# Optimization experiments

Measured on AMD Instinct MI355X. Metric: run time of the kernel, lower is better.

Reference implementation:

```python
import jax, jax.numpy as jnp
import numpy as np

B, NX, NT, W, M = 4, 512, 128, 64, 16
EPS = 1e-5


def setup_inputs() -> dict:
    key = jax.random.key(0)
    ks = jax.random.split(key, 13)
    scale = 1.0 / (W * W)  # torch: scale * torch.rand(..., cfloat) -> U[0,1) real & imag
    return {
        "x": jax.random.normal(ks[0], (B, NX, NT, W), jnp.float32),
        "grid": jnp.linspace(0.0, 1.0, NX, dtype=jnp.float32),
        "pole_re": scale * jax.random.uniform(ks[1], (W, W, M), jnp.float32),
        "pole_im": scale * jax.random.uniform(ks[2], (W, W, M), jnp.float32),
        "res_re": scale * jax.random.uniform(ks[3], (W, W, M), jnp.float32),
        "res_im": scale * jax.random.uniform(ks[4], (W, W, M), jnp.float32),
        "conv_w": jax.random.normal(ks[5], (W, W), jnp.float32) / np.sqrt(W),
        "conv_b": jax.random.normal(ks[6], (W,), jnp.float32) * 0.02,
        "gru_Wx": jax.random.normal(ks[7], (3 * W, W), jnp.float32) / np.sqrt(W),
        "gru_Wh": jax.random.normal(ks[8], (3 * W, W), jnp.float32) / np.sqrt(W),
        "gru_bx": jax.random.normal(ks[9], (3 * W,), jnp.float32) * 0.02,
        "gru_bh": jax.random.normal(ks[10], (3 * W,), jnp.float32) * 0.02,
        "out_W": jax.random.normal(ks[11], (W, W), jnp.float32) / np.sqrt(W),
        "out_b": jax.random.normal(ks[12], (W,), jnp.float32) * 0.02,
    }


def instance_norm(v):
    # torch InstanceNorm1d (affine=False, biased var) over last dim; v: [N, C, L]
    mu = v.mean(-1, keepdims=True)
    var = ((v - mu) ** 2).mean(-1, keepdims=True)
    return (v - mu) * jax.lax.rsqrt(var + EPS)


def pr_forward(xs, grid, pole, residue):
    # xs: [BT, W, Nx]; pole/residue: [in, out, modes] complex64
    nx = xs.shape[-1]
    dt = grid[1] - grid[0]
    alpha = jnp.fft.fft(xs)  # [BT, W, Nx] complex64
    lam = 1j * (2.0 * np.pi) * jnp.fft.fftfreq(nx, dt).astype(jnp.float32)  # [Nx]
    Hw = residue / (lam[:, None, None, None] - pole)  # [Nx, i, o, m]
    or1 = jnp.einsum('bix,xiom->box', alpha, Hw)       # [BT, W, Nx]
    or2 = -jnp.einsum('bix,xiom->bom', alpha, Hw)      # [BT, W, M]
    x1 = jnp.real(jnp.fft.ifft(or1, n=nx))
    # exp of outer product pole (x) grid: [i, o, m, Nx]
    term2 = jnp.exp(pole[..., None] * grid.astype(jnp.complex64)[None, None, None, :])
    # faithful to torch einsum 'bix,ioxz->boz': or2 channel contracts with term2's in-dim
    x2 = jnp.real(jnp.einsum('bim,iomz->boz', or2, term2)) / nx
    return x1 + x2


def gru(xseq, Wx, Wh, bx, bh):
    # xseq: [N, T, D] -> [N, T, H]; torch nn.GRU gate order (r, z, n)
    H = Wh.shape[1]
    gx = xseq @ Wx.T + bx  # precompute input gates [N, T, 3H]

    def step(h, g):
        gh = h @ Wh.T + bh
        xr, xz, xn = jnp.split(g, 3, axis=-1)
        hr, hz, hn = jnp.split(gh, 3, axis=-1)
        r = jax.nn.sigmoid(xr + hr)
        z = jax.nn.sigmoid(xz + hz)
        n = jnp.tanh(xn + r * hn)
        h = (1.0 - z) * n + z * h
        return h, h

    h0 = jnp.zeros((xseq.shape[0], H), xseq.dtype)
    _, hs = jax.lax.scan(step, h0, gx.transpose(1, 0, 2))
    return hs.transpose(1, 0, 2)


def reference(x, grid, pole_re, pole_im, res_re, res_im, conv_w, conv_b,
              gru_Wx, gru_Wh, gru_bx, gru_bh, out_W, out_b):
    b, nx, nt, w = x.shape
    xs = x.transpose(0, 2, 3, 1).reshape(b * nt, w, nx)  # [B*Nt, W, Nx]
    pole = pole_re + 1j * pole_im
    residue = res_re + 1j * res_im
    x1 = instance_norm(pr_forward(instance_norm(xs), grid, pole, residue))
    x2 = jnp.einsum('oi,bin->bon', conv_w, xs) + conv_b[None, :, None]  # Conv1d k=1
    h = jnp.sin(x1 + x2)
    h = h.reshape(b, nt, w, nx).transpose(0, 3, 1, 2).reshape(b * nx, nt, w)
    y = gru(h, gru_Wx, gru_Wh, gru_bx, gru_bh) @ out_W.T + out_b
    return y.reshape(b, nx, nt, w)
```

## Files before the change

### kernel.cpp

```cpp
#include <hip/hip_runtime.h>
#include <math.h>

#define PI2F 6.283185307179586f


__global__ __launch_bounds__(256) void k1a_transpose(const float* __restrict__ x,
                                                     float* __restrict__ xs) {
  const int bt = blockIdx.x >> 2, nt4 = blockIdx.x & 3;
  const int b = bt >> 7, t = bt & 127;
  const int n0 = nt4 * 128;
  __shared__ float tile[128 * 66];
  const int tid = threadIdx.x;
  const int i = tid & 63, nq = tid >> 6;
  const float* xb = x + (size_t)b * 4194304 + (size_t)t * 64;
  for (int k = 0; k < 32; k++) {
    int nl = nq + 4 * k;
    tile[nl * 66 + i] = xb[(size_t)(n0 + nl) * 8192 + i];
  }
  __syncthreads();
  float* dst = xs + (size_t)bt * 32768;
  for (int idx = tid; idx < 8192; idx += 256) {
    int ii = idx >> 7, nl = idx & 127;
    dst[ii * 512 + n0 + nl] = tile[nl * 66 + ii];
  }
}

__global__ __launch_bounds__(64) void k2_fft(const float* __restrict__ xs,
                                             float2* __restrict__ alpha,
                                             float2* __restrict__ a0,
                                             float2* __restrict__ a256,
                                             float2* __restrict__ s1o,
                                             float2* __restrict__ s2o,
                                             const float* __restrict__ grd) {
  __shared__ float2 bufA[512], bufB[512], tw[256];
  const int s = blockIdx.x, tid = threadIdx.x;
  const float dt = grd[1] - grd[0];
  const float Ndt = 512.f * dt;
  for (int m = tid; m < 256; m += 64) {
    float ang = -PI2F * (float)m * (1.f / 512.f);
    float sv, cv; sincosf(ang, &sv, &cv);
    tw[m].x = cv; tw[m].y = sv;
  }
  const float* src = xs + (size_t)s * 512;
  float v[8]; float sm = 0.f, sq = 0.f;
#pragma unroll
  for (int k = 0; k < 8; k++) { v[k] = src[tid + 64 * k]; sm += v[k]; sq += v[k] * v[k]; }
#pragma unroll
  for (int off = 32; off; off >>= 1) { sm += __shfl_down(sm, off); sq += __shfl_down(sq, off); }
  sm = __shfl(sm, 0); sq = __shfl(sq, 0);
  float mu = sm * (1.f / 512.f);
  float var = sq * (1.f / 512.f) - mu * mu;
  float rs = rsqrtf(var + 1e-5f);
#pragma unroll
  for (int k = 0; k < 8; k++) { bufA[tid + 64 * k].x = (v[k] - mu) * rs; bufA[tid + 64 * k].y = 0.f; }
  __syncthreads();
  float2* sp = bufA; float2* dp = bufB;
  int Ns = 1;
  for (int st = 0; st < 9; st++) {
    const int shift = 8 - st;
    for (int jj = 0; jj < 4; jj++) {
      int j = tid + 64 * jj;
      int r = j & (Ns - 1);
      float2 a = sp[j], b = sp[j + 256];
      float2 w = tw[r << shift];
      float wbx = w.x * b.x - w.y * b.y;
      float wby = w.x * b.y + w.y * b.x;
      int id = ((j >> st) << (st + 1)) + r;
      dp[id].x = a.x + wbx; dp[id].y = a.y + wby;
      dp[id + Ns].x = a.x - wbx; dp[id + Ns].y = a.y - wby;
    }
    __syncthreads();
    float2* tp = sp; sp = dp; dp = tp;
    Ns <<= 1;
  }
  float2* dst = alpha + (size_t)s * 256;
  float s1x = 0.f, s1y = 0.f, s2x = 0.f, s2y = 0.f;
  for (int k = tid; k < 512; k += 64) {
    float2 vv = sp[k];
    if (k < 256) dst[k] = vv;
    if (k != 0) {
      int kk = (k < 256) ? k : k - 512;
      float invL = Ndt / (PI2F * (float)kk);
      s1x += vv.y * invL; s1y -= vv.x * invL;
      float invL2 = invL * invL;
      s2x -= vv.x * invL2; s2y -= vv.y * invL2;
    }
  }
#pragma unroll
  for (int off = 32; off; off >>= 1) {
    s1x += __shfl_down(s1x, off); s1y += __shfl_down(s1y, off);
    s2x += __shfl_down(s2x, off); s2y += __shfl_down(s2y, off);
  }
  if (tid == 0) {
    s1o[s].x = s1x; s1o[s].y = s1y;
    s2o[s].x = s2x; s2o[s].y = s2y;
    a0[s] = sp[0];
    a256[s] = sp[256];
  }
}

__global__ __launch_bounds__(64) void k3a_R(const float* __restrict__ pre, const float* __restrict__ pim,
                                            const float* __restrict__ rre, const float* __restrict__ rim,
                                            float2* __restrict__ R0, float2* __restrict__ R1,
                                            float2* __restrict__ R2,
                                            float* __restrict__ Pm, float* __restrict__ Qm,
                                            float* __restrict__ ptr_re, float* __restrict__ ptr_im) {
  const int i = blockIdx.x, o = threadIdx.x;
  float r0x = 0, r0y = 0, r1x = 0, r1y = 0, r2x = 0, r2y = 0;
  for (int m = 0; m < 16; m++) {
    size_t idx = ((size_t)i * 64 + o) * 16 + m;
    float px = pre[idx], py = pim[idx];
    float rx = rre[idx], ry = rim[idx];
    r1x += rx; r1y += ry;
    r2x += rx * px - ry * py; r2y += rx * py + ry * px;
    float inv = 1.f / (px * px + py * py);
    r0x -= (rx * px + ry * py) * inv;
    r0y -= (ry * px - rx * py) * inv;
    ptr_re[((size_t)i * 16 + m) * 64 + o] = px;
    ptr_im[((size_t)i * 16 + m) * 64 + o] = py;
  }
  R0[i * 64 + o].x = r0x; R0[i * 64 + o].y = r0y;
  R1[i * 64 + o].x = r1x; R1[i * 64 + o].y = r1y;
  R2[i * 64 + o].x = r2x; R2[i * 64 + o].y = r2y;
  Pm[i * 64 + o] = 2.f * r1x;
  Qm[i * 64 + o] = 2.f * r2x;
}

__global__ __launch_bounds__(1024) void k3b_or2(const float* __restrict__ pre, const float* __restrict__ pim,
                                                const float* __restrict__ rre, const float* __restrict__ rim,
                                                const float2* __restrict__ a0, const float2* __restrict__ s1,
                                                const float2* __restrict__ s2, float2* __restrict__ or2) {
  const int bt = blockIdx.x;
  __shared__ float2 A0[64], S1[64], S2[64];
  const int tid = threadIdx.x;
  if (tid < 64) { A0[tid] = a0[bt * 64 + tid]; S1[tid] = s1[bt * 64 + tid]; S2[tid] = s2[bt * 64 + tid]; }
  __syncthreads();
  float ax = 0.f, ay = 0.f;
  for (int i = 0; i < 64; i++) {
    size_t idx = (size_t)i * 1024 + tid;
    float px = pre[idx], py = pim[idx];
    float rx = rre[idx], ry = rim[idx];
    float inv = 1.f / (px * px + py * py);
    float q0x = -(rx * px + ry * py) * inv;
    float q0y = -(ry * px - rx * py) * inv;
    float2 a0v = A0[i], s1v = S1[i], s2v = S2[i];
    float tx = q0x * a0v.x - q0y * a0v.y + rx * s1v.x - ry * s1v.y;
    float ty = q0x * a0v.y + q0y * a0v.x + rx * s1v.y + ry * s1v.x;
    float rpx = rx * px - ry * py, rpy = rx * py + ry * px;
    tx += rpx * s2v.x - rpy * s2v.y;
    ty += rpx * s2v.y + rpy * s2v.x;
    ax -= tx; ay -= ty;
  }
  or2[(size_t)bt * 1024 + tid].x = ax;
  or2[(size_t)bt * 1024 + tid].y = ay;
}

__global__ __launch_bounds__(256) void k3c_T(const float2* __restrict__ or2,
                                             const float* __restrict__ ptr_re, const float* __restrict__ ptr_im,
                                             const float2* __restrict__ R0, const float2* __restrict__ R1,
                                             const float2* __restrict__ R2,
                                             const float2* __restrict__ a0, const float2* __restrict__ a256,
                                             float* __restrict__ T0, float* __restrict__ T1,
                                             float* __restrict__ T2,
                                             float* __restrict__ or10re, float* __restrict__ r256o,
                                             const float* __restrict__ grd) {
  const int bt = blockIdx.x * 4 + (threadIdx.x >> 6);
  const int o = threadIdx.x & 63;
  const float dt = grd[1] - grd[0];
  const float invL256 = -(512.f * dt) / (PI2F * 256.f);
  float ox = 0.f;
  float c1x = 0.f, c1y = 0.f, c2x = 0.f, c2y = 0.f;
  for (int i = 0; i < 64; i++) {
    float2 av = a0[bt * 64 + i];
    float2 rv = R0[i * 64 + o];
    ox += av.x * rv.x - av.y * rv.y;
    float2 aw = a256[bt * 64 + i];
    float2 r1v = R1[i * 64 + o], r2v = R2[i * 64 + o];
    c1x += aw.x * r1v.x - aw.y * r1v.y;
    c1y += aw.x * r1v.y + aw.y * r1v.x;
    c2x += aw.x * r2v.x - aw.y * r2v.y;
    c2y += aw.x * r2v.y + aw.y * r2v.x;
  }
  or10re[bt * 64 + o] = ox;
  r256o[bt * 64 + o] = invL256 * (c1y - invL256 * c2x);
  float t0 = 0.f, t1 = 0.f, t2 = 0.f;
  for (int im = 0; im < 1024; im++) {
    float2 c = or2[(size_t)bt * 1024 + im];
    float px = ptr_re[(size_t)im * 64 + o], py = ptr_im[(size_t)im * 64 + o];
    t0 += c.x;
    t1 += c.x * px - c.y * py;
    float p2x = px * px - py * py, p2y = 2.f * px * py;
    t2 += c.x * p2x - c.y * p2y;
  }
  T1[bt * 64 + o] = t1; T2[bt * 64 + o] = t2;
  if (o == 0) T0[bt] = t0;
}

__global__ __launch_bounds__(256) void k4_or1(float2* __restrict__ alpha,
                                              const float* __restrict__ Pm, const float* __restrict__ Qm,
                                              const float* __restrict__ or10re, const float* __restrict__ r256o,
                                              const float* __restrict__ grd) {
  const int bt = blockIdx.x >> 2, xc = blockIdx.x & 3;
  const int x0 = xc * 64;
  __shared__ float aRe[64][68], aIm[64][68];
  const int tid = threadIdx.x;
  const float dt = grd[1] - grd[0];
  const float Ndt = 512.f * dt;
  float2* base = alpha + (size_t)bt * 16384;
  for (int idx = tid; idx < 4096; idx += 256) {
    int ii = idx >> 6, xl = idx & 63;
    float2 v = base[ii * 256 + x0 + xl];
    aRe[ii][xl] = v.x; aIm[ii][xl] = v.y;
  }
  __syncthreads();
  const int xq = tid & 15, oq = tid >> 4;
  const int xb = xq * 4, ob = oq * 4;
  float c1r[4][4] = {}, c1i[4][4] = {}, c2r[4][4] = {}, c2i[4][4] = {};
#pragma unroll 4
  for (int i = 0; i < 64; i++) {
    float4 ar = *(const float4*)&aRe[i][xb];
    float4 ai = *(const float4*)&aIm[i][xb];
    float4 pv = *(const float4*)&Pm[i * 64 + ob];
    float4 qv = *(const float4*)&Qm[i * 64 + ob];
    float pa[4] = {pv.x, pv.y, pv.z, pv.w};
    float qa[4] = {qv.x, qv.y, qv.z, qv.w};
    float arr[4] = {ar.x, ar.y, ar.z, ar.w};
    float aii[4] = {ai.x, ai.y, ai.z, ai.w};
#pragma unroll
    for (int a = 0; a < 4; a++) {
#pragma unroll
      for (int c = 0; c < 4; c++) {
        c1r[a][c] += arr[c] * pa[a];
        c1i[a][c] += aii[c] * pa[a];
        c2r[a][c] += arr[c] * qa[a];
        c2i[a][c] += aii[c] * qa[a];
      }
    }
  }
#pragma unroll
  for (int a = 0; a < 4; a++) {
    int o = ob + a;
    float2* orow = base + o * 256 + x0;
#pragma unroll
    for (int c = 0; c < 4; c++) {
      int gx = x0 + xb + c;
      float re, im;
      if (gx == 0) {
        re = or10re[bt * 64 + o];
        im = r256o[bt * 64 + o];
      } else {
        float invL = Ndt / (PI2F * (float)gx);
        re = invL * (c1i[a][c] - invL * c2r[a][c]);
        im = -invL * (c1r[a][c] + invL * c2i[a][c]);
      }
      orow[xb + c].x = re; orow[xb + c].y = im;
    }
  }
}

__global__ __launch_bounds__(64) void k5_ifft(const float2* __restrict__ G,
                                              float* __restrict__ x1,
                                              const float* __restrict__ T0, const float* __restrict__ T1,
                                              const float* __restrict__ T2, const float* __restrict__ grd) {
  __shared__ float2 bufA[512], bufB[512], tw[256];
  const int s = blockIdx.x, tid = threadIdx.x;
  const int bt = s >> 6;
  for (int m = tid; m < 256; m += 64) {
    float ang = PI2F * (float)m * (1.f / 512.f);
    float sv, cv; sincosf(ang, &sv, &cv);
    tw[m].x = cv; tw[m].y = sv;
  }
  const float2* src = G + (size_t)s * 256;
  float2 g0 = src[0];
  for (int k = tid; k < 512; k += 64) {
    float2 vv; vv.x = 0.f; vv.y = 0.f;
    if (k >= 1 && k < 256) vv = src[k];
    bufA[k] = vv;
  }
  __syncthreads();
  float2* sp = bufA; float2* dp = bufB;
  int Ns = 1;
  for (int st = 0; st < 9; st++) {
    const int shift = 8 - st;
    for (int jj = 0; jj < 4; jj++) {
      int j = tid + 64 * jj;
      int r = j & (Ns - 1);
      float2 a = sp[j], b = sp[j + 256];
      float2 w = tw[r << shift];
      float wbx = w.x * b.x - w.y * b.y;
      float wby = w.x * b.y + w.y * b.x;
      int id = ((j >> st) << (st + 1)) + r;
      dp[id].x = a.x + wbx; dp[id].y = a.y + wby;
      dp[id + Ns].x = a.x - wbx; dp[id + Ns].y = a.y - wby;
    }
    __syncthreads();
    float2* tp = sp; sp = dp; dp = tp;
    Ns <<= 1;
  }
  const float t0 = T0[bt], t1 = T1[s], t2 = T2[s];
  float* dst = x1 + (size_t)s * 512;
  for (int k = tid; k < 512; k += 64) {
    float g = grd[k];
    float sgn = (k & 1) ? -1.f : 1.f;
    dst[k] = (sp[k].x + g0.x + sgn * g0.y + t0 + t1 * g + 0.5f * t2 * g * g) * (1.f / 512.f);
  }
}

__global__ __launch_bounds__(256) void k6a_stats(const float* __restrict__ x1,
                                                 float* __restrict__ mu2, float* __restrict__ rs2) {
  const int row = blockIdx.x * 4 + (threadIdx.x >> 6);
  const int lane = threadIdx.x & 63;
  const float* p = x1 + (size_t)row * 512;
  float s = 0.f, s2 = 0.f;
#pragma unroll
  for (int k = 0; k < 8; k++) { float v = p[lane + 64 * k]; s += v; s2 += v * v; }
#pragma unroll
  for (int off = 32; off; off >>= 1) { s += __shfl_down(s, off); s2 += __shfl_down(s2, off); }
  if (lane == 0) {
    float mu = s * (1.f / 512.f);
    float var = s2 * (1.f / 512.f) - mu * mu;
    mu2[row] = mu;
    rs2[row] = rsqrtf(var + 1e-5f);
  }
}

__global__ __launch_bounds__(256) void k6b_assemble(const float* __restrict__ xsraw,
                                                    const float* __restrict__ x1,
                                                    const float* __restrict__ conv_w,
                                                    const float* __restrict__ conv_b,
                                                    const float* __restrict__ mu2, const float* __restrict__ rs2,
                                                    float* __restrict__ hseq) {
  const int bt = blockIdx.x >> 2, nt4 = blockIdx.x & 3;
  const int b = bt >> 7, t = bt & 127;
  const int n0 = nt4 * 128;
  __shared__ float xt[128 * 66];
  __shared__ float wt[64 * 66];
  __shared__ float mun[64], rsn[64];
  const int tid = threadIdx.x;
  for (int idx = tid; idx < 4096; idx += 256) {
    int o = idx >> 6, ii = idx & 63;
    wt[o * 66 + ii] = conv_w[idx];
  }
  if (tid < 64) { mun[tid] = mu2[bt * 64 + tid]; rsn[tid] = rs2[bt * 64 + tid]; }
  const float* src = xsraw + (size_t)bt * 32768;
  for (int idx = tid; idx < 8192; idx += 256) {
    int ii = idx >> 7, nl = idx & 127;
    xt[nl * 66 + ii] = src[ii * 512 + n0 + nl];
  }
  __syncthreads();
  const int lane = tid & 63, og = tid >> 6;
  float acc[2][16];
  for (int half = 0; half < 2; half++) {
    int nl = lane + 64 * half;
#pragma unroll
    for (int j = 0; j < 16; j++) acc[half][j] = conv_b[og * 16 + j];
    const float2* xrow = (const float2*)&xt[nl * 66];
#pragma unroll 4
    for (int i2 = 0; i2 < 32; i2++) {
      float2 v = xrow[i2];
#pragma unroll
      for (int j = 0; j < 16; j++) {
        float2 wv = *(const float2*)&wt[(og * 16 + j) * 66 + 2 * i2];
        acc[half][j] += wv.x * v.x + wv.y * v.y;
      }
    }
  }
  const float* xb = x1 + (size_t)bt * 32768 + n0;
  for (int half = 0; half < 2; half++) {
    int nl = lane + 64 * half;
#pragma unroll
    for (int j = 0; j < 16; j++) {
      int o = og * 16 + j;
      float v = (xb[o * 512 + nl] - mun[o]) * rsn[o] + acc[half][j];
      acc[half][j] = sinf(v);
    }
  }
  __syncthreads();
  float* tile = xt;
  for (int half = 0; half < 2; half++) {
    int nl = lane + 64 * half;
#pragma unroll
    for (int j = 0; j < 16; j++) tile[(og * 16 + j) * 129 + nl] = acc[half][j];
  }
  __syncthreads();
  for (int idx = tid; idx < 8192; idx += 256) {
    int nl = idx >> 6, o = idx & 63;
    hseq[(((size_t)(b * 512 + n0 + nl)) * 128 + t) * 64 + o] = tile[o * 129 + nl];
  }
}

__global__ __launch_bounds__(64, 1) void k7_gru(const float* __restrict__ hseq,
                                                const float* __restrict__ Wx, const float* __restrict__ Wh,
                                                const float* __restrict__ bx, const float* __restrict__ bh,
                                                float* __restrict__ hist) {
  __shared__ float hx[128];
  const int row = blockIdx.x;
  const int j = threadIdx.x;
  float wxr[64], wxz[64], wxn[64], whr[64], whz[64], whn[64];
  {
    const float4* pr = (const float4*)(Wx + (size_t)j * 64);
    const float4* pz = (const float4*)(Wx + (size_t)(j + 64) * 64);
    const float4* pn = (const float4*)(Wx + (size_t)(j + 128) * 64);
    const float4* qr = (const float4*)(Wh + (size_t)j * 64);
    const float4* qz = (const float4*)(Wh + (size_t)(j + 64) * 64);
    const float4* qn = (const float4*)(Wh + (size_t)(j + 128) * 64);
#pragma unroll
    for (int c4 = 0; c4 < 16; c4++) {
      float4 v;
      v = pr[c4]; wxr[4*c4]=v.x; wxr[4*c4+1]=v.y; wxr[4*c4+2]=v.z; wxr[4*c4+3]=v.w;
      v = pz[c4]; wxz[4*c4]=v.x; wxz[4*c4+1]=v.y; wxz[4*c4+2]=v.z; wxz[4*c4+3]=v.w;
      v = pn[c4]; wxn[4*c4]=v.x; wxn[4*c4+1]=v.y; wxn[4*c4+2]=v.z; wxn[4*c4+3]=v.w;
      v = qr[c4]; whr[4*c4]=v.x; whr[4*c4+1]=v.y; whr[4*c4+2]=v.z; whr[4*c4+3]=v.w;
      v = qz[c4]; whz[4*c4]=v.x; whz[4*c4+1]=v.y; whz[4*c4+2]=v.z; whz[4*c4+3]=v.w;
      v = qn[c4]; whn[4*c4]=v.x; whn[4*c4+1]=v.y; whn[4*c4+2]=v.z; whn[4*c4+3]=v.w;
    }
  }
  const float br  = bx[j] + bh[j];
  const float bz  = bx[j + 64] + bh[j + 64];
  const float bxn = bx[j + 128];
  const float bhn = bh[j + 128];
  const float* xrow = hseq + (size_t)row * 8192;
  float* hrow = hist + (size_t)row * 8192;
  float h = 0.f;
  float xcur = xrow[j];
  for (int t = 0; t < 128; t++) {
    float xnext = (t < 127) ? xrow[(t + 1) * 64 + j] : 0.f;
    __syncthreads();
    hx[j] = h;
    hx[64 + j] = xcur;
    __syncthreads();
    float aR = br, aZ = bz, aXN = bxn, aHN = bhn;
#pragma unroll
    for (int c4 = 0; c4 < 16; c4++) {
      float4 hv = *(const float4*)&hx[c4 * 4];
      float4 xv = *(const float4*)&hx[64 + c4 * 4];
      aR  += whr[4*c4] * hv.x + whr[4*c4+1] * hv.y + whr[4*c4+2] * hv.z + whr[4*c4+3] * hv.w;
      aZ  += whz[4*c4] * hv.x + whz[4*c4+1] * hv.y + whz[4*c4+2] * hv.z + whz[4*c4+3] * hv.w;
      aHN += whn[4*c4] * hv.x + whn[4*c4+1] * hv.y + whn[4*c4+2] * hv.z + whn[4*c4+3] * hv.w;
      aR  += wxr[4*c4] * xv.x + wxr[4*c4+1] * xv.y + wxr[4*c4+2] * xv.z + wxr[4*c4+3] * xv.w;
      aZ  += wxz[4*c4] * xv.x + wxz[4*c4+1] * xv.y + wxz[4*c4+2] * xv.z + wxz[4*c4+3] * xv.w;
      aXN += wxn[4*c4] * xv.x + wxn[4*c4+1] * xv.y + wxn[4*c4+2] * xv.z + wxn[4*c4+3] * xv.w;
    }
    float r = 1.f / (1.f + __expf(-aR));
    float z = 1.f / (1.f + __expf(-aZ));
    float nv = aXN + r * aHN;
    float e2 = __expf(2.f * nv);
    float th = 1.f - 2.f / (e2 + 1.f);
    h = (1.f - z) * th + z * h;
    hrow[t * 64 + j] = h;
    xcur = xnext;
  }
}

__global__ __launch_bounds__(256) void k8_out(const float* __restrict__ hist,
                                              const float* __restrict__ outW, const float* __restrict__ outb,
                                              float* __restrict__ y) {
  __shared__ float ht[64 * 68];
  __shared__ float wl[4096];
  const int tid = threadIdx.x;
  const int rt0 = blockIdx.x * 64;
  for (int idx = tid; idx < 4096; idx += 256) wl[idx] = outW[idx];
  for (int idx = tid; idx < 4096; idx += 256) {
    int rt = idx >> 6, c = idx & 63;
    ht[rt * 68 + c] = hist[(size_t)(rt0 + rt) * 64 + c];
  }
  __syncthreads();
  const int j = tid & 63, rg = tid >> 6;
  float wj[64];
#pragma unroll
  for (int c = 0; c < 64; c++) wj[c] = wl[j * 64 + c];
  const float bj = outb[j];
  for (int k = 0; k < 16; k++) {
    int rt = rg + 4 * k;
    float acc = bj;
    const float4* hp = (const float4*)&ht[rt * 68];
#pragma unroll
    for (int c4 = 0; c4 < 16; c4++) {
      float4 hv = hp[c4];
      acc += wj[4 * c4] * hv.x + wj[4 * c4 + 1] * hv.y + wj[4 * c4 + 2] * hv.z + wj[4 * c4 + 3] * hv.w;
    }
    y[(size_t)(rt0 + rt) * 64 + j] = acc;
  }
}

extern "C" void kernel_launch(void* const* d_in, const int* in_sizes, int n_in,
                              void* d_out, int out_size, void* d_ws, size_t ws_size,
                              hipStream_t stream) {
  (void)in_sizes; (void)n_in; (void)out_size;
  const float* x      = (const float*)d_in[0];
  const float* grd    = (const float*)d_in[1];
  const float* pre    = (const float*)d_in[2];
  const float* pim    = (const float*)d_in[3];
  const float* rre    = (const float*)d_in[4];
  const float* rim    = (const float*)d_in[5];
  const float* conv_w = (const float*)d_in[6];
  const float* conv_b = (const float*)d_in[7];
  const float* gWx    = (const float*)d_in[8];
  const float* gWh    = (const float*)d_in[9];
  const float* gbx    = (const float*)d_in[10];
  const float* gbh    = (const float*)d_in[11];
  const float* outW   = (const float*)d_in[12];
  const float* outb   = (const float*)d_in[13];
  float* out = (float*)d_out;
  float* ws  = (float*)d_ws;

  if (ws_size < 52003328ULL * 4ULL) return;

  float*  XS = ws;
  float2* AH = (float2*)(ws + 16777216);
  float*  X1 = ws + 33554432;
  float*  sm = ws + 50331648;
  float2* A0    = (float2*)(sm + 0);
  float2* A256  = (float2*)(sm + 65536);
  float2* S1    = (float2*)(sm + 131072);
  float2* S2    = (float2*)(sm + 196608);
  float2* R0    = (float2*)(sm + 262144);
  float2* R1C   = (float2*)(sm + 270336);
  float2* R2C   = (float2*)(sm + 278528);
  float*  Pm    = sm + 286720;
  float*  Qm    = sm + 290816;
  float*  PTR   = sm + 294912;
  float*  PTI   = sm + 360448;
  float2* OR2   = (float2*)(sm + 425984);
  float*  T0    = sm + 1474560;
  float*  T1    = sm + 1475072;
  float*  T2    = sm + 1507840;
  float*  OR10R = sm + 1540608;
  float*  R256  = sm + 1573376;
  float*  MU2   = sm + 1606144;
  float*  RS2   = sm + 1638912;

  float* hseq = (float*)AH;
  float* hist = X1;

  k1a_transpose<<<2048, 256, 0, stream>>>(x, XS);
  k2_fft<<<32768, 64, 0, stream>>>(XS, AH, A0, A256, S1, S2, grd);
  k3a_R<<<64, 64, 0, stream>>>(pre, pim, rre, rim, R0, R1C, R2C, Pm, Qm, PTR, PTI);
  k3b_or2<<<512, 1024, 0, stream>>>(pre, pim, rre, rim, A0, S1, S2, OR2);
  k3c_T<<<128, 256, 0, stream>>>(OR2, PTR, PTI, R0, R1C, R2C, A0, A256, T0, T1, T2, OR10R, R256, grd);
  k4_or1<<<2048, 256, 0, stream>>>(AH, Pm, Qm, OR10R, R256, grd);
  k5_ifft<<<32768, 64, 0, stream>>>(AH, X1, T0, T1, T2, grd);
  k6a_stats<<<8192, 256, 0, stream>>>(X1, MU2, RS2);
  k6b_assemble<<<2048, 256, 0, stream>>>(XS, X1, conv_w, conv_b, MU2, RS2, hseq);
  k7_gru<<<2048, 64, 0, stream>>>(hseq, gWx, gWh, gbx, gbh, hist);
  k8_out<<<4096, 256, 0, stream>>>(hist, outW, outb, out);
}
```

Baseline: 1.235 ms.

## Hoist GRU input projection into a separate batched GEMM with bf16 intermediates

Moves the GRU input-gate projection (x·Wx + bx) out of the sequential recurrence into a new parallel kernel that computes all time steps at once. The results are stored as bf16 gate buffers, and the hidden sequence itself is also stored as bf16. The recurrent kernel now keeps only Wh in registers, which halves register pressure, lets launch bounds allow two blocks per CU, and shortens the serial per-step chain. This costs an extra kernel, extra memory traffic for the three gate buffers, and some precision because bf16 is used for activations that were fp32.

```diff
diff --git a/kernel.cpp b/kernel.cpp
--- a/kernel.cpp
+++ b/kernel.cpp
@@ -2,6 +2,16 @@
 #include <math.h>
 
 #define PI2F 6.283185307179586f
+typedef unsigned short ushort_t;
+
+__device__ inline ushort_t f2bf(float f) {
+  unsigned u = __float_as_uint(f);
+  unsigned r = (u + 0x7FFFu + ((u >> 16) & 1u)) >> 16;
+  return (ushort_t)r;
+}
+__device__ inline float bf2f(ushort_t u) {
+  return __uint_as_float(((unsigned)u) << 16);
+}
 
 
 __global__ __launch_bounds__(256) void k1a_transpose(const float* __restrict__ x,
@@ -329,7 +339,7 @@
                                                     const float* __restrict__ conv_w,
                                                     const float* __restrict__ conv_b,
                                                     const float* __restrict__ mu2, const float* __restrict__ rs2,
-                                                    float* __restrict__ hseq) {
+                                                    ushort_t* __restrict__ hseqb) {
   const int bt = blockIdx.x >> 2, nt4 = blockIdx.x & 3;
   const int b = bt >> 7, t = bt & 127;
   const int n0 = nt4 * 128;
@@ -385,70 +395,111 @@
   __syncthreads();
   for (int idx = tid; idx < 8192; idx += 256) {
     int nl = idx >> 6, o = idx & 63;
-    hseq[(((size_t)(b * 512 + n0 + nl)) * 128 + t) * 64 + o] = tile[o * 129 + nl];
-  }
-}
-
-__global__ __launch_bounds__(64, 1) void k7_gru(const float* __restrict__ hseq,
-                                                const float* __restrict__ Wx, const float* __restrict__ Wh,
-                                                const float* __restrict__ bx, const float* __restrict__ bh,
+    hseqb[(((size_t)(b * 512 + n0 + nl)) * 128 + t) * 64 + o] = f2bf(tile[o * 129 + nl]);
+  }
+}
+
+__global__ __launch_bounds__(256) void k6c_xgemm(const ushort_t* __restrict__ hseqb,
+                                                 const float* __restrict__ Wx, const float* __restrict__ bxv,
+                                                 ushort_t* __restrict__ gxr, ushort_t* __restrict__ gxz,
+                                                 ushort_t* __restrict__ gxn) {
+  __shared__ float ht[64][68];
+  __shared__ float wt[192][66];
+  const int tid = threadIdx.x;
+  const size_t rt0 = (size_t)blockIdx.x * 64;
+  for (int idx = tid; idx < 12288; idx += 256) {
+    int g = idx >> 6, c = idx & 63;
+    wt[g][c] = Wx[idx];
+  }
+  for (int idx = tid; idx < 4096; idx += 256) {
+    int rt = idx >> 6, c = idx & 63;
+    ht[rt][c] = bf2f(hseqb[(rt0 + rt) * 64 + c]);
+  }
+  __syncthreads();
+  const int a = tid & 15, bq = tid >> 4;
+  float acc[4][12];
+#pragma unroll
+  for (int g = 0; g < 12; g++) {
+    float bv = bxv[bq * 12 + g];
+    acc[0][g] = bv; acc[1][g] = bv; acc[2][g] = bv; acc[3][g] = bv;
+  }
+  for (int c4 = 0; c4 < 16; c4++) {
+    float4 h0 = *(const float4*)&ht[a][c4 * 4];
+    float4 h1 = *(const float4*)&ht[a + 16][c4 * 4];
+    float4 h2 = *(const float4*)&ht[a + 32][c4 * 4];
+    float4 h3 = *(const float4*)&ht[a + 48][c4 * 4];
+#pragma unroll
+    for (int g = 0; g < 12; g++) {
+      float4 wv = *(const float4*)&wt[bq * 12 + g][c4 * 4];
+      acc[0][g] += h0.x * wv.x + h0.y * wv.y + h0.z * wv.z + h0.w * wv.w;
+      acc[1][g] += h1.x * wv.x + h1.y * wv.y + h1.z * wv.z + h1.w * wv.w;
+      acc[2][g] += h2.x * wv.x + h2.y * wv.y + h2.z * wv.z + h2.w * wv.w;
+      acc[3][g] += h3.x * wv.x + h3.y * wv.y + h3.z * wv.z + h3.w * wv.w;
+    }
+  }
+#pragma unroll
+  for (int r = 0; r < 4; r++) {
+    size_t rt = rt0 + a + 16 * r;
+#pragma unroll
+    for (int g = 0; g < 12; g++) {
+      int gg = bq * 12 + g;
+      ushort_t v = f2bf(acc[r][g]);
+      ushort_t* dst = (gg < 64) ? gxr : ((gg < 128) ? gxz : gxn);
+      dst[rt * 64 + (gg & 63)] = v;
+    }
+  }
+}
+
+__global__ __launch_bounds__(64, 2) void k7_gru(const ushort_t* __restrict__ gxr,
+                                                const ushort_t* __restrict__ gxz,
+                                                const ushort_t* __restrict__ gxn,
+                                                const float* __restrict__ Wh,
+                                                const float* __restrict__ bh,
                                                 float* __restrict__ hist) {
-  __shared__ float hx[128];
+  __shared__ float hx[64];
   const int row = blockIdx.x;
   const int j = threadIdx.x;
-  float wxr[64], wxz[64], wxn[64], whr[64], whz[64], whn[64];
+  float whr[64], whz[64], whn[64];
   {
-    const float4* pr = (const float4*)(Wx + (size_t)j * 64);
-    const float4* pz = (const float4*)(Wx + (size_t)(j + 64) * 64);
-    const float4* pn = (const float4*)(Wx + (size_t)(j + 128) * 64);
     const float4* qr = (const float4*)(Wh + (size_t)j * 64);
     const float4* qz = (const float4*)(Wh + (size_t)(j + 64) * 64);
     const float4* qn = (const float4*)(Wh + (size_t)(j + 128) * 64);
 #pragma unroll
     for (int c4 = 0; c4 < 16; c4++) {
       float4 v;
-      v = pr[c4]; wxr[4*c4]=v.x; wxr[4*c4+1]=v.y; wxr[4*c4+2]=v.z; wxr[4*c4+3]=v.w;
-      v = pz[c4]; wxz[4*c4]=v.x; wxz[4*c4+1]=v.y; wxz[4*c4+2]=v.z; wxz[4*c4+3]=v.w;
-      v = pn[c4]; wxn[4*c4]=v.x; wxn[4*c4+1]=v.y; wxn[4*c4+2]=v.z; wxn[4*c4+3]=v.w;
       v = qr[c4]; whr[4*c4]=v.x; whr[4*c4+1]=v.y; whr[4*c4+2]=v.z; whr[4*c4+3]=v.w;
       v = qz[c4]; whz[4*c4]=v.x; whz[4*c4+1]=v.y; whz[4*c4+2]=v.z; whz[4*c4+3]=v.w;
       v = qn[c4]; whn[4*c4]=v.x; whn[4*c4+1]=v.y; whn[4*c4+2]=v.z; whn[4*c4+3]=v.w;
     }
   }
-  const float br  = bx[j] + bh[j];
-  const float bz  = bx[j + 64] + bh[j + 64];
-  const float bxn = bx[j + 128];
-  const float bhn = bh[j + 128];
-  const float* xrow = hseq + (size_t)row * 8192;
+  const float bhr = bh[j], bhz = bh[j + 64], bhn = bh[j + 128];
+  const ushort_t* gr = gxr + (size_t)row * 8192;
+  const ushort_t* gz = gxz + (size_t)row * 8192;
+  const ushort_t* gn = gxn + (size_t)row * 8192;
   float* hrow = hist + (size_t)row * 8192;
   float h = 0.f;
-  float xcur = xrow[j];
   for (int t = 0; t < 128; t++) {
-    float xnext = (t < 127) ? xrow[(t + 1) * 64 + j] : 0.f;
+    float xr = bf2f(gr[t * 64 + j]);
+    float xz = bf2f(gz[t * 64 + j]);
+    float xn = bf2f(gn[t * 64 + j]);
     __syncthreads();
     hx[j] = h;
-    hx[64 + j] = xcur;
     __syncthreads();
-    float aR = br, aZ = bz, aXN = bxn, aHN = bhn;
+    float aR = bhr, aZ = bhz, aN = bhn;
 #pragma unroll
     for (int c4 = 0; c4 < 16; c4++) {
       float4 hv = *(const float4*)&hx[c4 * 4];
-      float4 xv = *(const float4*)&hx[64 + c4 * 4];
-      aR  += whr[4*c4] * hv.x + whr[4*c4+1] * hv.y + whr[4*c4+2] * hv.z + whr[4*c4+3] * hv.w;
-      aZ  += whz[4*c4] * hv.x + whz[4*c4+1] * hv.y + whz[4*c4+2] * hv.z + whz[4*c4+3] * hv.w;
-      aHN += whn[4*c4] * hv.x + whn[4*c4+1] * hv.y + whn[4*c4+2] * hv.z + whn[4*c4+3] * hv.w;
-      aR  += wxr[4*c4] * xv.x + wxr[4*c4+1] * xv.y + wxr[4*c4+2] * xv.z + wxr[4*c4+3] * xv.w;
-      aZ  += wxz[4*c4] * xv.x + wxz[4*c4+1] * xv.y + wxz[4*c4+2] * xv.z + wxz[4*c4+3] * xv.w;
-      aXN += wxn[4*c4] * xv.x + wxn[4*c4+1] * xv.y + wxn[4*c4+2] * xv.z + wxn[4*c4+3] * xv.w;
-    }
-    float r = 1.f / (1.f + __expf(-aR));
-    float z = 1.f / (1.f + __expf(-aZ));
-    float nv = aXN + r * aHN;
+      aR += whr[4*c4] * hv.x + whr[4*c4+1] * hv.y + whr[4*c4+2] * hv.z + whr[4*c4+3] * hv.w;
+      aZ += whz[4*c4] * hv.x + whz[4*c4+1] * hv.y + whz[4*c4+2] * hv.z + whz[4*c4+3] * hv.w;
+      aN += whn[4*c4] * hv.x + whn[4*c4+1] * hv.y + whn[4*c4+2] * hv.z + whn[4*c4+3] * hv.w;
+    }
+    float r = 1.f / (1.f + __expf(-(xr + aR)));
+    float z = 1.f / (1.f + __expf(-(xz + aZ)));
+    float nv = xn + r * aN;
     float e2 = __expf(2.f * nv);
     float th = 1.f - 2.f / (e2 + 1.f);
     h = (1.f - z) * th + z * h;
     hrow[t * 64 + j] = h;
-    xcur = xnext;
   }
 }
 
@@ -530,7 +581,10 @@
   float*  MU2   = sm + 1606144;
   float*  RS2   = sm + 1638912;
 
-  float* hseq = (float*)AH;
+  ushort_t* hseqb = (ushort_t*)AH;
+  ushort_t* GXN   = (ushort_t*)AH + 16777216;
+  ushort_t* GXR   = (ushort_t*)XS;
+  ushort_t* GXZ   = (ushort_t*)XS + 16777216;
   float* hist = X1;
 
   k1a_transpose<<<2048, 256, 0, stream>>>(x, XS);
@@ -541,7 +595,8 @@
   k4_or1<<<2048, 256, 0, stream>>>(AH, Pm, Qm, OR10R, R256, grd);
   k5_ifft<<<32768, 64, 0, stream>>>(AH, X1, T0, T1, T2, grd);
   k6a_stats<<<8192, 256, 0, stream>>>(X1, MU2, RS2);
-  k6b_assemble<<<2048, 256, 0, stream>>>(XS, X1, conv_w, conv_b, MU2, RS2, hseq);
-  k7_gru<<<2048, 64, 0, stream>>>(hseq, gWx, gWh, gbx, gbh, hist);
+  k6b_assemble<<<2048, 256, 0, stream>>>(XS, X1, conv_w, conv_b, MU2, RS2, hseqb);
+  k6c_xgemm<<<4096, 256, 0, stream>>>(hseqb, gWx, gbx, GXR, GXZ, GXN);
+  k7_gru<<<2048, 64, 0, stream>>>(GXR, GXZ, GXN, gWh, gbh, hist);
   k8_out<<<4096, 256, 0, stream>>>(hist, outW, outb, out);
 }
```

Result: faster. 1.178 ms (-4.6%).
